# Performance work log

Hardware: AMD Instinct MI355X
Metric: run time of the kernel (lower is better)

The kernel has to match this reference:

```python
import jax, jax.numpy as jnp
import numpy as np

DIM = 4096
N_HEADS = 32
N_KV_HEADS = 8
HEAD_DIM = 128
EPS = 1e-6
SEQ = 2048
N_SEG = 4
SEG_LEN = SEQ // N_SEG


def setup_inputs() -> dict:
    key = jax.random.key(0)
    ks = jax.random.split(key, 6)
    s = 0.02
    x = jax.random.normal(ks[0], (1, SEQ, DIM), jnp.float32)
    wq = jax.random.normal(ks[1], (N_HEADS * HEAD_DIM, DIM), jnp.float32) * s
    wk = jax.random.normal(ks[2], (N_KV_HEADS * HEAD_DIM, DIM), jnp.float32) * s
    wv = jax.random.normal(ks[3], (N_KV_HEADS * HEAD_DIM, DIM), jnp.float32) * s
    wo = jax.random.normal(ks[4], (DIM, N_HEADS * HEAD_DIM), jnp.float32) * s
    q_norm_w = jnp.ones((HEAD_DIM,), jnp.float32)
    k_norm_w = jnp.ones((HEAD_DIM,), jnp.float32)
    # RoPE cache: [max_pos, head_dim//2, 2] = (cos, sin)
    inv_freq = 1.0 / (10000.0 ** (jnp.arange(0, HEAD_DIM // 2, dtype=jnp.float32) / (HEAD_DIM // 2)))
    t = jnp.arange(SEQ, dtype=jnp.float32)
    freqs = jnp.outer(t, inv_freq)  # [SEQ, hd/2]
    rope_cache = jnp.stack([jnp.cos(freqs), jnp.sin(freqs)], axis=-1)
    # packed varlen: 4 segments of 512, positions restart per segment
    positions = (jnp.arange(SEQ, dtype=jnp.int32) % SEG_LEN)[None, :]
    cu_seqlens = jnp.arange(N_SEG + 1, dtype=jnp.int32) * SEG_LEN
    return {"x": x, "wq": wq, "wk": wk, "wv": wv, "wo": wo,
            "q_norm_w": q_norm_w, "k_norm_w": k_norm_w,
            "rope_cache": rope_cache, "positions": positions,
            "cu_seqlens": cu_seqlens}


def _rms_norm(x, w):
    xf = x.astype(jnp.float32)
    var = jnp.mean(xf * xf, axis=-1, keepdims=True)
    return w * (xf * jax.lax.rsqrt(var + EPS))


def _apply_rope(x, rope_cache, positions):
    # x: [bs, S, h, hd]; rope_cache: [P, hd/2, 2]; positions: [bs, S]
    cs = rope_cache[positions]                    # [bs, S, hd/2, 2]
    cos = cs[..., 0][:, :, None, :]               # [bs, S, 1, hd/2]
    sin = cs[..., 1][:, :, None, :]
    half = x.shape[-1] // 2
    x1, x2 = x[..., :half], x[..., half:]
    return jnp.concatenate([x1 * cos - x2 * sin, x2 * cos + x1 * sin], axis=-1)


def reference(x, wq, wk, wv, wo, q_norm_w, k_norm_w, rope_cache, positions, cu_seqlens):
    bs, S, _ = x.shape
    n_rep = N_HEADS // N_KV_HEADS
    xq = (x @ wq.T).reshape(bs, S, N_HEADS, HEAD_DIM)
    xk = (x @ wk.T).reshape(bs, S, N_KV_HEADS, HEAD_DIM)
    xv = (x @ wv.T).reshape(bs, S, N_KV_HEADS, HEAD_DIM)
    xq = _rms_norm(xq, q_norm_w)
    xk = _rms_norm(xk, k_norm_w)
    xq = _apply_rope(xq, rope_cache, positions)
    xk = _apply_rope(xk, rope_cache, positions)
    # GQA: repeat kv heads
    xk = jnp.repeat(xk, n_rep, axis=2)
    xv = jnp.repeat(xv, n_rep, axis=2)
    q = xq.transpose(0, 2, 1, 3)  # [bs, h, S, hd]
    k = xk.transpose(0, 2, 1, 3)
    v = xv.transpose(0, 2, 1, 3)
    # varlen mask: causal within each packed segment
    idx = jnp.arange(S)
    seg = jnp.searchsorted(cu_seqlens, idx, side='right') - 1  # [S]
    mask = (seg[:, None] == seg[None, :]) & (idx[:, None] >= idx[None, :])
    scale = HEAD_DIM ** -0.5
    scores = jnp.einsum('bhqd,bhkd->bhqk', q, k) * scale
    scores = jnp.where(mask[None, None], scores, jnp.float32(-1e30))
    probs = jax.nn.softmax(scores, axis=-1)
    out = jnp.einsum('bhqk,bhkd->bhqd', probs, v)
    out = out.transpose(0, 2, 1, 3).reshape(bs, S, N_HEADS * HEAD_DIM)
    return out @ wo.T
```

## Files before the change

### kernel.cpp

```cpp
#include <hip/hip_runtime.h>

typedef __bf16 bf16_t;
typedef __bf16 bf16x8 __attribute__((ext_vector_type(8)));
typedef __bf16 bf16x4 __attribute__((ext_vector_type(4)));
typedef float f32x4 __attribute__((ext_vector_type(4)));

#define SEQL 2048
#define DIMM 4096
#define NH 32
#define NKV 8
#define HD 128

__device__ __forceinline__ void gl2lds16(const void* g, void* l) {
  __builtin_amdgcn_global_load_lds((__attribute__((address_space(1))) void*)g,
                                   (__attribute__((address_space(3))) void*)l,
                                   16, 0, 0);
}

__global__ __launch_bounds__(256) void cvt5_kernel(const float* __restrict__ s0,
                                                   const float* __restrict__ s1,
                                                   const float* __restrict__ s2,
                                                   const float* __restrict__ s3,
                                                   const float* __restrict__ s4,
                                                   bf16_t* __restrict__ dst) {
  const long base = (long)blockIdx.x * 4096;
  const float* s;
  long o;
  if (base < 8388608L)       { s = s0; o = base; }
  else if (base < 25165824L) { s = s1; o = base - 8388608L; }
  else if (base < 29360128L) { s = s2; o = base - 25165824L; }
  else if (base < 33554432L) { s = s3; o = base - 29360128L; }
  else                       { s = s4; o = base - 33554432L; }
  const long t4 = threadIdx.x * 4;
#pragma unroll
  for (int j = 0; j < 4; ++j) {
    const long e = t4 + j * 1024;
    float4 v = *(const float4*)(s + o + e);
    bf16x4 ov;
    ov[0] = (bf16_t)v.x; ov[1] = (bf16_t)v.y; ov[2] = (bf16_t)v.z; ov[3] = (bf16_t)v.w;
    *(bf16x4*)(dst + base + e) = ov;
  }
}

#define BK2 32
#define EPS 264
#define QSCALE (0.08838834764831845f * 1.4426950408889634f)
__global__ __launch_bounds__(512, 2) void gemm_qkv8(const bf16_t* __restrict__ A,
                                                    const bf16_t* __restrict__ B,
                                                    const float* __restrict__ qnw,
                                                    const float* __restrict__ knw,
                                                    const float* __restrict__ rope,
                                                    const int* __restrict__ pos,
                                                    bf16_t* __restrict__ Qb,
                                                    bf16_t* __restrict__ Kb,
                                                    bf16_t* __restrict__ Vb) {
  __shared__ __align__(16) bf16_t smem[65536];
  const int K = DIMM;
  const int NT = K / BK2;
  const int tid = threadIdx.x;
  const int lin = blockIdx.x;
  const int xcd = lin & 7, idx = lin >> 3;
  const int bm = (idx & 7) * 256;
  const int bn = ((idx >> 3) + xcd * 3) * 256;
  const int lane = tid & 63, wave = tid >> 6;
  const int wrow = wave >> 2, wcol = wave & 3;
  const int wm = wrow * 128, wn = wcol * 64;
  const int lr = lane & 15, quad = lane >> 4;
  const int swz = (quad ^ ((lr >> 1) & 3)) << 3;

  long asrc[2]; int adst[2];
#pragma unroll
  for (int c = 0; c < 2; ++c) {
    const int id = tid + 512 * c;
    asrc[c] = (long)(id >> 2) * K + (long)((((id & 3) ^ ((id >> 3) & 3)) << 3));
    adst[c] = id * 8;
  }
  const bf16_t* Abase = A + (long)bm * K;
  const bf16_t* Bbase = B + (long)bn * K;

  f32x4 acc[8][4];
#pragma unroll
  for (int mi = 0; mi < 8; ++mi)
#pragma unroll
    for (int ni = 0; ni < 4; ++ni)
      acc[mi][ni] = (f32x4){0.f, 0.f, 0.f, 0.f};

#define STAGE(t, c)                                                              \
  do {                                                                           \
    const int slot_ = (t) & 3;                                                   \
    const long k0_ = (long)(t) * BK2;                                            \
    gl2lds16(Abase + asrc[c] + k0_, smem + slot_ * 8192 + adst[c]);              \
    gl2lds16(Bbase + asrc[c] + k0_, smem + 32768 + slot_ * 8192 + adst[c]);      \
  } while (0)

  STAGE(0, 0); STAGE(0, 1); STAGE(1, 0); STAGE(1, 1);
  asm volatile("s_waitcnt vmcnt(4)" ::: "memory");
  __builtin_amdgcn_s_barrier();

  for (int t = 0; t < NT; ++t) {
    const bf16_t* As = smem + (t & 3) * 8192;
    const bf16_t* Bs = smem + 32768 + (t & 3) * 8192;
    bf16x8 af[4], bfr[4];
#pragma unroll
    for (int mi = 0; mi < 4; ++mi)
      af[mi] = *(const bf16x8*)&As[(wm + mi * 16 + lr) * 32 + swz];
#pragma unroll
    for (int ni = 0; ni < 4; ++ni)
      bfr[ni] = *(const bf16x8*)&Bs[(wn + ni * 16 + lr) * 32 + swz];
    if (t + 2 < NT) STAGE(t + 2, 0);
    __builtin_amdgcn_s_barrier();
    asm volatile("s_waitcnt lgkmcnt(0)" ::: "memory");
    __builtin_amdgcn_sched_barrier(0);
    __builtin_amdgcn_s_setprio(1);
#pragma unroll
    for (int mi = 0; mi < 4; ++mi)
#pragma unroll
      for (int ni = 0; ni < 4; ++ni)
        acc[mi][ni] = __builtin_amdgcn_mfma_f32_16x16x32_bf16(af[mi], bfr[ni], acc[mi][ni], 0, 0, 0);
    __builtin_amdgcn_s_setprio(0);
    __builtin_amdgcn_s_barrier();
#pragma unroll
    for (int mi = 0; mi < 4; ++mi)
      af[mi] = *(const bf16x8*)&As[(wm + 64 + mi * 16 + lr) * 32 + swz];
    if (t + 2 < NT) STAGE(t + 2, 1);
    __builtin_amdgcn_s_barrier();
    asm volatile("s_waitcnt lgkmcnt(0)" ::: "memory");
    __builtin_amdgcn_sched_barrier(0);
    __builtin_amdgcn_s_setprio(1);
#pragma unroll
    for (int mi = 0; mi < 4; ++mi)
#pragma unroll
      for (int ni = 0; ni < 4; ++ni)
        acc[4 + mi][ni] = __builtin_amdgcn_mfma_f32_16x16x32_bf16(af[mi], bfr[ni], acc[4 + mi][ni], 0, 0, 0);
    __builtin_amdgcn_s_setprio(0);
    if (t + 2 < NT) { asm volatile("s_waitcnt vmcnt(4)" ::: "memory"); }
    else            { asm volatile("s_waitcnt vmcnt(0)" ::: "memory"); }
    __builtin_amdgcn_s_barrier();
  }
#undef STAGE

  const bool isQ = bn < 4096;
  const bool isV = bn >= 5120;
#pragma unroll 1
  for (int half = 0; half < 2; ++half) {
    __syncthreads();
    if (wrow == half) {
#pragma unroll
      for (int mi = 0; mi < 8; ++mi)
#pragma unroll
        for (int ni = 0; ni < 4; ++ni)
#pragma unroll
          for (int r = 0; r < 4; ++r)
            smem[(mi * 16 + quad * 4 + r) * EPS + wn + ni * 16 + lr] = (bf16_t)acc[mi][ni][r];
    }
    __syncthreads();
    const int growb = bm + half * 128;
    if (!isV) {
      const int r = tid >> 2, hh = (tid >> 1) & 1, hf = tid & 1;
      const int cb = bn + hh * 128;
      const float* nwp = isQ ? qnw : knw;
      const float osc = isQ ? QSCALE : 1.0f;
      bf16_t* outp = isQ ? (Qb + (long)(cb >> 7) * SEQL * HD)
                         : (Kb + (long)((cb - 4096) >> 7) * SEQL * HD);
      bf16x8 rowv[16];
#pragma unroll
      for (int j = 0; j < 16; ++j) rowv[j] = *(const bf16x8*)&smem[r * EPS + hh * 128 + j * 8];
      float ss = 0.f;
#pragma unroll
      for (int j = 0; j < 16; ++j)
#pragma unroll
        for (int e = 0; e < 8; ++e) { const float f = (float)rowv[j][e]; ss += f * f; }
      const float sc = rsqrtf(ss * (1.0f / 128.0f) + 1e-6f) * osc;
      const int p = pos[growb + r];
      const float* rp = rope + p * 128;
      bf16_t obuf[64];
#pragma unroll
      for (int g = 0; g < 8; ++g) {
#pragma unroll
        for (int e = 0; e < 8; ++e) {
          const int i = g * 8 + e;
          const float2 cs = *(const float2*)(rp + 2 * i);
          const float nlo = (float)rowv[i >> 3][i & 7] * sc * nwp[i];
          const float nhi = (float)rowv[8 + (i >> 3)][i & 7] * sc * nwp[64 + i];
          obuf[i] = (bf16_t)(hf ? (nhi * cs.x + nlo * cs.y) : (nlo * cs.x - nhi * cs.y));
        }
      }
      bf16_t* op = outp + (long)(growb + r) * HD + hf * 64;
#pragma unroll
      for (int g = 0; g < 8; ++g) *(bf16x8*)(op + g * 8) = *(const bf16x8*)&obuf[g * 8];
    } else {
      const int d = tid & 127, q2 = tid >> 7;
      const int hh = q2 >> 1, shalf = q2 & 1;
      const int hv = ((bn - 5120) >> 7) + hh;
      bf16_t* vp = Vb + ((long)hv * HD + d) * SEQL + growb + shalf * 64;
#pragma unroll
      for (int grp = 0; grp < 8; ++grp) {
        bf16x8 tv;
#pragma unroll
        for (int e = 0; e < 8; ++e) tv[e] = smem[(shalf * 64 + grp * 8 + e) * EPS + hh * 128 + d];
        *(bf16x8*)(vp + grp * 8) = tv;
      }
    }
  }
}

template <typename CT>
__global__ __launch_bounds__(256, 3) void gemm_bt_kernel(const bf16_t* __restrict__ A,
                                                         const bf16_t* __restrict__ B,
                                                         CT* __restrict__ C,
                                                         int N, int K, int npanel) {
  __shared__ bf16_t lA[128 * 64];
  __shared__ bf16_t lB[128 * 64];
  const int tid = threadIdx.x;
  const int lin = blockIdx.x;
  const int xcd = lin & 7, idx = lin >> 3;
  const int bm = (idx & 15) * 128;
  const int bn = ((idx >> 4) + xcd * npanel) * 128;
  const int lane = tid & 63, wave = tid >> 6;
  const int wm = (wave >> 1) * 64, wn = (wave & 1) * 64;
  const int lr = lane & 15, quad = lane >> 4;

  f32x4 acc[4][4];
#pragma unroll
  for (int mi = 0; mi < 4; ++mi)
#pragma unroll
    for (int ni = 0; ni < 4; ++ni)
      acc[mi][ni] = (f32x4){0.f, 0.f, 0.f, 0.f};

  long soff[4];
#pragma unroll
  for (int c = 0; c < 4; ++c) {
    const int s = tid + 256 * c;
    soff[c] = (long)(s >> 3) * K + (((s & 7) ^ ((s >> 3) & 7)) << 3);
  }
  const bf16_t* Abase = A + (long)bm * K;
  const bf16_t* Bbase = B + (long)bn * K;

  for (int k0 = 0; k0 < K; k0 += 64) {
    __syncthreads();
#pragma unroll
    for (int c = 0; c < 4; ++c) {
      gl2lds16(Abase + soff[c] + k0, lA + (tid + 256 * c) * 8);
      gl2lds16(Bbase + soff[c] + k0, lB + (tid + 256 * c) * 8);
    }
    __syncthreads();
#pragma unroll
    for (int ks = 0; ks < 2; ++ks) {
      bf16x8 af[4], bfr[4];
#pragma unroll
      for (int mi = 0; mi < 4; ++mi)
        af[mi] = *(const bf16x8*)&lA[(wm + mi * 16 + lr) * 64 + ((((ks << 2) | quad) ^ (lr & 7)) << 3)];
#pragma unroll
      for (int ni = 0; ni < 4; ++ni)
        bfr[ni] = *(const bf16x8*)&lB[(wn + ni * 16 + lr) * 64 + ((((ks << 2) | quad) ^ (lr & 7)) << 3)];
#pragma unroll
      for (int mi = 0; mi < 4; ++mi)
#pragma unroll
        for (int ni = 0; ni < 4; ++ni)
          acc[mi][ni] = __builtin_amdgcn_mfma_f32_16x16x32_bf16(af[mi], bfr[ni], acc[mi][ni], 0, 0, 0);
    }
  }

#pragma unroll
  for (int mi = 0; mi < 4; ++mi) {
    const int row = bm + wm + mi * 16 + quad * 4;
#pragma unroll
    for (int ni = 0; ni < 4; ++ni) {
      const int col = bn + wn + ni * 16 + lr;
      CT* cp = C + (long)row * N + col;
#pragma unroll
      for (int r = 0; r < 4; ++r) cp[(long)r * N] = (CT)acc[mi][ni][r];
    }
  }
}

#define CK 64
#define PSTR 72
__global__ __launch_bounds__(256) void attn_kernel(const bf16_t* __restrict__ Q,
                                                   const bf16_t* __restrict__ Kt,
                                                   const bf16_t* __restrict__ Vt,
                                                   bf16_t* __restrict__ O) {
  __shared__ bf16_t lK[CK * 128];
  __shared__ bf16_t lV[144 * CK];
  __shared__ bf16_t lP[128 * PSTR];
  const int lin = blockIdx.x;
  const int qb = (lin < 256) ? (3 - (lin & 1)) : (lin & 1);
  const int gh = (lin >> 1) & 127;
  const int h = gh & 31, g = gh >> 5;
  const int hk = h >> 2;
  const int tid = threadIdx.x, lane = tid & 63, wave = tid >> 6;
  const int lr = lane & 15, quad = lane >> 4;
  const int s_base = g * 512 + qb * 128;

  if (tid < 128) {
    bf16x8 one8;
#pragma unroll
    for (int j = 0; j < 8; ++j) one8[j] = (bf16_t)1.0f;
    *(bf16x8*)&lV[128 * CK + tid * 8] = one8;
  }

  bf16x8 qf[2][4];
  const bf16_t* Qp = Q + ((long)h * SEQL + s_base + wave * 32 + lr) * HD + quad * 8;
#pragma unroll
  for (int mi = 0; mi < 2; ++mi)
#pragma unroll
    for (int ks = 0; ks < 4; ++ks)
      qf[mi][ks] = *(const bf16x8*)(Qp + mi * 16 * HD + ks * 32);

  f32x4 oacc[2][9];
#pragma unroll
  for (int mi = 0; mi < 2; ++mi)
#pragma unroll
    for (int di = 0; di < 9; ++di) oacc[mi][di] = (f32x4){0.f, 0.f, 0.f, 0.f};

  const int nchunk = 2 * qb + 2;
  for (int c = 0; c < nchunk; ++c) {
    __syncthreads();
    {
      const bf16_t* Kg = Kt + ((long)hk * SEQL + g * 512 + c * CK) * HD;
      const bf16_t* Vg = Vt + (long)hk * HD * SEQL + g * 512 + c * CK;
#pragma unroll
      for (int cc = 0; cc < 4; ++cc) {
        const int i = tid + 256 * cc;
        gl2lds16(Kg + (long)(i >> 4) * HD + (i & 15) * 8, lK + i * 8);
        gl2lds16(Vg + (long)(i >> 3) * SEQL + (i & 7) * 8, lV + i * 8);
      }
    }
    __syncthreads();

    f32x4 sv[2][4];
#pragma unroll
    for (int mi = 0; mi < 2; ++mi)
#pragma unroll
      for (int ni = 0; ni < 4; ++ni) sv[mi][ni] = (f32x4){0.f, 0.f, 0.f, 0.f};
#pragma unroll
    for (int ks = 0; ks < 4; ++ks) {
#pragma unroll
      for (int ni = 0; ni < 4; ++ni) {
        const bf16x8 kf = *(const bf16x8*)&lK[(ni * 16 + lr) * 128 + ks * 32 + quad * 8];
        sv[0][ni] = __builtin_amdgcn_mfma_f32_16x16x32_bf16(qf[0][ks], kf, sv[0][ni], 0, 0, 0);
        sv[1][ni] = __builtin_amdgcn_mfma_f32_16x16x32_bf16(qf[1][ks], kf, sv[1][ni], 0, 0, 0);
      }
    }

#pragma unroll
    for (int mi = 0; mi < 2; ++mi)
#pragma unroll
      for (int ni = 0; ni < 4; ++ni)
#pragma unroll
        for (int r = 0; r < 4; ++r) {
          const int colseg = c * CK + ni * 16 + lr;
          const int rowseg = qb * 128 + wave * 32 + mi * 16 + quad * 4 + r;
          float p = exp2f(sv[mi][ni][r]);
          p = (colseg > rowseg) ? 0.f : p;
          lP[(wave * 32 + mi * 16 + quad * 4 + r) * PSTR + ni * 16 + lr] = (bf16_t)p;
        }
    __syncthreads();

#pragma unroll
    for (int ks = 0; ks < 2; ++ks) {
      const bf16x8 pf0 = *(const bf16x8*)&lP[(wave * 32 + lr) * PSTR + ks * 32 + quad * 8];
      const bf16x8 pf1 = *(const bf16x8*)&lP[(wave * 32 + 16 + lr) * PSTR + ks * 32 + quad * 8];
#pragma unroll
      for (int di = 0; di < 9; ++di) {
        const bf16x8 vfr = *(const bf16x8*)&lV[(di * 16 + lr) * CK + ks * 32 + quad * 8];
        oacc[0][di] = __builtin_amdgcn_mfma_f32_16x16x32_bf16(pf0, vfr, oacc[0][di], 0, 0, 0);
        oacc[1][di] = __builtin_amdgcn_mfma_f32_16x16x32_bf16(pf1, vfr, oacc[1][di], 0, 0, 0);
      }
    }
  }

#pragma unroll
  for (int mi = 0; mi < 2; ++mi)
#pragma unroll
    for (int r = 0; r < 4; ++r) {
      const float inv = 1.0f / oacc[mi][8][r];
      const int row = s_base + wave * 32 + mi * 16 + quad * 4 + r;
      bf16_t* opp = O + (long)row * DIMM + h * HD + lr;
#pragma unroll
      for (int di = 0; di < 8; ++di) opp[di * 16] = (bf16_t)(oacc[mi][di][r] * inv);
    }
}

extern "C" void kernel_launch(void* const* d_in, const int* in_sizes, int n_in,
                              void* d_out, int out_size, void* d_ws, size_t ws_size,
                              hipStream_t stream) {
  (void)in_sizes; (void)n_in; (void)out_size; (void)ws_size;
  const float* x    = (const float*)d_in[0];
  const float* wq   = (const float*)d_in[1];
  const float* wk   = (const float*)d_in[2];
  const float* wv   = (const float*)d_in[3];
  const float* wo   = (const float*)d_in[4];
  const float* qnw  = (const float*)d_in[5];
  const float* knw  = (const float*)d_in[6];
  const float* rope = (const float*)d_in[7];
  const int*   pos  = (const int*)d_in[8];
  float* out = (float*)d_out;

  char* ws = (char*)d_ws;
  size_t off = 0;
  auto alloc = [&](size_t b) { char* p = ws + off; off += (b + 255) & ~(size_t)255; return p; };
  bf16_t* xb    = (bf16_t*)alloc((size_t)SEQL * DIMM * 2);
  bf16_t* wqkvb = (bf16_t*)alloc((size_t)DIMM * DIMM * 2);
  alloc((size_t)NKV * HD * DIMM * 2);
  alloc((size_t)NKV * HD * DIMM * 2);
  bf16_t* wob   = (bf16_t*)alloc((size_t)DIMM * DIMM * 2);
  bf16_t* Qb    = (bf16_t*)alloc((size_t)NH * SEQL * HD * 2);
  bf16_t* Kb    = (bf16_t*)alloc((size_t)NKV * SEQL * HD * 2);
  bf16_t* Vb    = (bf16_t*)alloc((size_t)NKV * SEQL * HD * 2);
  bf16_t* attnb = xb;

  cvt5_kernel<<<dim3(12288), 256, 0, stream>>>(x, wq, wk, wv, wo, xb);
  gemm_qkv8<<<dim3(192), 512, 0, stream>>>(xb, wqkvb, qnw, knw, rope, pos, Qb, Kb, Vb);
  attn_kernel<<<dim3(512), 256, 0, stream>>>(Qb, Kb, Vb, attnb);
  gemm_bt_kernel<float><<<dim3(512), 256, 0, stream>>>(attnb, wob, out, DIMM, DIMM, 4);
}
```

Before: 531.1 us.

## Retile fused QKV GEMM to 128x384 blocks for full CU occupancy

Changes the fused QKV projection tile from 256x256 to 128x384, which raises the grid from 192 to 256 blocks so every CU gets work on a 256-CU part. It reworks the LDS staging split, wave tiling and the normalize/RoPE epilogue to match: the epilogue now writes all accumulators at once and handles three 128-wide head groups in two passes. The intent is to remove the partially idle wave of blocks. The trade-off is lower arithmetic intensity per tile and a less balanced second epilogue pass.

```diff
diff --git a/kernel.cpp b/kernel.cpp
--- a/kernel.cpp
+++ b/kernel.cpp
@@ -43,7 +43,7 @@
 }
 
 #define BK2 32
-#define EPS 264
+#define EPSTR 392
 #define QSCALE (0.08838834764831845f * 1.4426950408889634f)
 __global__ __launch_bounds__(512, 2) void gemm_qkv8(const bf16_t* __restrict__ A,
                                                     const bf16_t* __restrict__ B,
@@ -60,54 +60,64 @@
   const int tid = threadIdx.x;
   const int lin = blockIdx.x;
   const int xcd = lin & 7, idx = lin >> 3;
-  const int bm = (idx & 7) * 256;
-  const int bn = ((idx >> 3) + xcd * 3) * 256;
+  const int bm = (idx & 15) * 128;
+  const int bn = ((idx >> 4) + xcd * 2) * 384;
   const int lane = tid & 63, wave = tid >> 6;
   const int wrow = wave >> 2, wcol = wave & 3;
-  const int wm = wrow * 128, wn = wcol * 64;
+  const int wm = wrow * 64, wn = wcol * 96;
   const int lr = lane & 15, quad = lane >> 4;
   const int swz = (quad ^ ((lr >> 1) & 3)) << 3;
 
-  long asrc[2]; int adst[2];
-#pragma unroll
-  for (int c = 0; c < 2; ++c) {
+  const int idA = tid;
+  const long srcA = (long)(idA >> 2) * K + (((idA & 3) ^ ((idA >> 3) & 3)) << 3);
+  const int dstA = idA * 8;
+  long srcB[3]; int dstB[3];
+#pragma unroll
+  for (int c = 0; c < 3; ++c) {
     const int id = tid + 512 * c;
-    asrc[c] = (long)(id >> 2) * K + (long)((((id & 3) ^ ((id >> 3) & 3)) << 3));
-    adst[c] = id * 8;
+    srcB[c] = (long)(id >> 2) * K + (((id & 3) ^ ((id >> 3) & 3)) << 3);
+    dstB[c] = id * 8;
   }
   const bf16_t* Abase = A + (long)bm * K;
   const bf16_t* Bbase = B + (long)bn * K;
 
-  f32x4 acc[8][4];
-#pragma unroll
-  for (int mi = 0; mi < 8; ++mi)
-#pragma unroll
-    for (int ni = 0; ni < 4; ++ni)
+  f32x4 acc[4][6];
+#pragma unroll
+  for (int mi = 0; mi < 4; ++mi)
+#pragma unroll
+    for (int ni = 0; ni < 6; ++ni)
       acc[mi][ni] = (f32x4){0.f, 0.f, 0.f, 0.f};
 
-#define STAGE(t, c)                                                              \
+#define STAGE_A(t)                                                               \
   do {                                                                           \
-    const int slot_ = (t) & 3;                                                   \
+    const int sl_ = (t) & 3;                                                     \
     const long k0_ = (long)(t) * BK2;                                            \
-    gl2lds16(Abase + asrc[c] + k0_, smem + slot_ * 8192 + adst[c]);              \
-    gl2lds16(Bbase + asrc[c] + k0_, smem + 32768 + slot_ * 8192 + adst[c]);      \
+    gl2lds16(Abase + srcA + k0_, smem + sl_ * 4096 + dstA);                      \
+    gl2lds16(Bbase + srcB[0] + k0_, smem + 16384 + sl_ * 12288 + dstB[0]);       \
   } while (0)
-
-  STAGE(0, 0); STAGE(0, 1); STAGE(1, 0); STAGE(1, 1);
+#define STAGE_B(t)                                                               \
+  do {                                                                           \
+    const int sl_ = (t) & 3;                                                     \
+    const long k0_ = (long)(t) * BK2;                                            \
+    gl2lds16(Bbase + srcB[1] + k0_, smem + 16384 + sl_ * 12288 + dstB[1]);       \
+    gl2lds16(Bbase + srcB[2] + k0_, smem + 16384 + sl_ * 12288 + dstB[2]);       \
+  } while (0)
+
+  STAGE_A(0); STAGE_B(0); STAGE_A(1); STAGE_B(1);
   asm volatile("s_waitcnt vmcnt(4)" ::: "memory");
   __builtin_amdgcn_s_barrier();
 
   for (int t = 0; t < NT; ++t) {
-    const bf16_t* As = smem + (t & 3) * 8192;
-    const bf16_t* Bs = smem + 32768 + (t & 3) * 8192;
-    bf16x8 af[4], bfr[4];
+    const bf16_t* As = smem + (t & 3) * 4096;
+    const bf16_t* Bs = smem + 16384 + (t & 3) * 12288;
+    bf16x8 af[4], bfr[6];
 #pragma unroll
     for (int mi = 0; mi < 4; ++mi)
       af[mi] = *(const bf16x8*)&As[(wm + mi * 16 + lr) * 32 + swz];
 #pragma unroll
-    for (int ni = 0; ni < 4; ++ni)
+    for (int ni = 0; ni < 3; ++ni)
       bfr[ni] = *(const bf16x8*)&Bs[(wn + ni * 16 + lr) * 32 + swz];
-    if (t + 2 < NT) STAGE(t + 2, 0);
+    if (t + 2 < NT) STAGE_A(t + 2);
     __builtin_amdgcn_s_barrier();
     asm volatile("s_waitcnt lgkmcnt(0)" ::: "memory");
     __builtin_amdgcn_sched_barrier(0);
@@ -115,14 +125,14 @@
 #pragma unroll
     for (int mi = 0; mi < 4; ++mi)
 #pragma unroll
-      for (int ni = 0; ni < 4; ++ni)
+      for (int ni = 0; ni < 3; ++ni)
         acc[mi][ni] = __builtin_amdgcn_mfma_f32_16x16x32_bf16(af[mi], bfr[ni], acc[mi][ni], 0, 0, 0);
     __builtin_amdgcn_s_setprio(0);
     __builtin_amdgcn_s_barrier();
 #pragma unroll
-    for (int mi = 0; mi < 4; ++mi)
-      af[mi] = *(const bf16x8*)&As[(wm + 64 + mi * 16 + lr) * 32 + swz];
-    if (t + 2 < NT) STAGE(t + 2, 1);
+    for (int ni = 3; ni < 6; ++ni)
+      bfr[ni] = *(const bf16x8*)&Bs[(wn + ni * 16 + lr) * 32 + swz];
+    if (t + 2 < NT) STAGE_B(t + 2);
     __builtin_amdgcn_s_barrier();
     asm volatile("s_waitcnt lgkmcnt(0)" ::: "memory");
     __builtin_amdgcn_sched_barrier(0);
@@ -130,74 +140,75 @@
 #pragma unroll
     for (int mi = 0; mi < 4; ++mi)
 #pragma unroll
-      for (int ni = 0; ni < 4; ++ni)
-        acc[4 + mi][ni] = __builtin_amdgcn_mfma_f32_16x16x32_bf16(af[mi], bfr[ni], acc[4 + mi][ni], 0, 0, 0);
+      for (int ni = 3; ni < 6; ++ni)
+        acc[mi][ni] = __builtin_amdgcn_mfma_f32_16x16x32_bf16(af[mi], bfr[ni], acc[mi][ni], 0, 0, 0);
     __builtin_amdgcn_s_setprio(0);
     if (t + 2 < NT) { asm volatile("s_waitcnt vmcnt(4)" ::: "memory"); }
     else            { asm volatile("s_waitcnt vmcnt(0)" ::: "memory"); }
     __builtin_amdgcn_s_barrier();
   }
-#undef STAGE
-
-  const bool isQ = bn < 4096;
-  const bool isV = bn >= 5120;
+#undef STAGE_A
+#undef STAGE_B
+
+  __syncthreads();
+#pragma unroll
+  for (int mi = 0; mi < 4; ++mi)
+#pragma unroll
+    for (int ni = 0; ni < 6; ++ni)
+#pragma unroll
+      for (int r = 0; r < 4; ++r)
+        smem[(wm + mi * 16 + quad * 4 + r) * EPSTR + wn + ni * 16 + lr] = (bf16_t)acc[mi][ni][r];
+  __syncthreads();
+
 #pragma unroll 1
-  for (int half = 0; half < 2; ++half) {
-    __syncthreads();
-    if (wrow == half) {
-#pragma unroll
-      for (int mi = 0; mi < 8; ++mi)
-#pragma unroll
-        for (int ni = 0; ni < 4; ++ni)
-#pragma unroll
-          for (int r = 0; r < 4; ++r)
-            smem[(mi * 16 + quad * 4 + r) * EPS + wn + ni * 16 + lr] = (bf16_t)acc[mi][ni][r];
-    }
-    __syncthreads();
-    const int growb = bm + half * 128;
-    if (!isV) {
-      const int r = tid >> 2, hh = (tid >> 1) & 1, hf = tid & 1;
-      const int cb = bn + hh * 128;
+  for (int pass = 0; pass < 2; ++pass) {
+    const int hh = (pass == 0) ? (tid >> 8) : 2;
+    if (pass == 1 && tid >= 256) break;
+    const int tl = tid & 255;
+    const int col0 = bn + hh * 128;
+    if (col0 < 5120) {
+      const bool isQ = col0 < 4096;
+      const int r = tl >> 1, hf = tl & 1;
+      const bf16_t* rowp = smem + r * EPSTR + hh * 128;
+      float ss = 0.f;
+#pragma unroll
+      for (int j = 0; j < 16; ++j) {
+        const bf16x8 v = *(const bf16x8*)&rowp[j * 8];
+#pragma unroll
+        for (int e = 0; e < 8; ++e) { const float f = (float)v[e]; ss += f * f; }
+      }
+      const float sc = rsqrtf(ss * (1.0f / 128.0f) + 1e-6f) * (isQ ? QSCALE : 1.0f);
       const float* nwp = isQ ? qnw : knw;
-      const float osc = isQ ? QSCALE : 1.0f;
-      bf16_t* outp = isQ ? (Qb + (long)(cb >> 7) * SEQL * HD)
-                         : (Kb + (long)((cb - 4096) >> 7) * SEQL * HD);
-      bf16x8 rowv[16];
-#pragma unroll
-      for (int j = 0; j < 16; ++j) rowv[j] = *(const bf16x8*)&smem[r * EPS + hh * 128 + j * 8];
-      float ss = 0.f;
-#pragma unroll
-      for (int j = 0; j < 16; ++j)
-#pragma unroll
-        for (int e = 0; e < 8; ++e) { const float f = (float)rowv[j][e]; ss += f * f; }
-      const float sc = rsqrtf(ss * (1.0f / 128.0f) + 1e-6f) * osc;
-      const int p = pos[growb + r];
+      const int p = pos[bm + r];
       const float* rp = rope + p * 128;
-      bf16_t obuf[64];
+      bf16_t* op = (isQ ? (Qb + (long)(col0 >> 7) * SEQL * HD)
+                        : (Kb + (long)((col0 - 4096) >> 7) * SEQL * HD))
+                   + (long)(bm + r) * HD + hf * 64;
 #pragma unroll
       for (int g = 0; g < 8; ++g) {
+        const bf16x8 lo = *(const bf16x8*)&rowp[g * 8];
+        const bf16x8 hi = *(const bf16x8*)&rowp[64 + g * 8];
+        bf16x8 ov;
 #pragma unroll
         for (int e = 0; e < 8; ++e) {
           const int i = g * 8 + e;
           const float2 cs = *(const float2*)(rp + 2 * i);
-          const float nlo = (float)rowv[i >> 3][i & 7] * sc * nwp[i];
-          const float nhi = (float)rowv[8 + (i >> 3)][i & 7] * sc * nwp[64 + i];
-          obuf[i] = (bf16_t)(hf ? (nhi * cs.x + nlo * cs.y) : (nlo * cs.x - nhi * cs.y));
+          const float nlo = (float)lo[e] * sc * nwp[i];
+          const float nhi = (float)hi[e] * sc * nwp[64 + i];
+          ov[e] = (bf16_t)(hf ? (nhi * cs.x + nlo * cs.y) : (nlo * cs.x - nhi * cs.y));
         }
-      }
-      bf16_t* op = outp + (long)(growb + r) * HD + hf * 64;
-#pragma unroll
-      for (int g = 0; g < 8; ++g) *(bf16x8*)(op + g * 8) = *(const bf16x8*)&obuf[g * 8];
+        *(bf16x8*)(op + g * 8) = ov;
+      }
     } else {
-      const int d = tid & 127, q2 = tid >> 7;
-      const int hh = q2 >> 1, shalf = q2 & 1;
-      const int hv = ((bn - 5120) >> 7) + hh;
-      bf16_t* vp = Vb + ((long)hv * HD + d) * SEQL + growb + shalf * 64;
+      const int d = tl & 127, shalf = tl >> 7;
+      const int hv = (col0 - 5120) >> 7;
+      bf16_t* vp = Vb + ((long)hv * HD + d) * SEQL + bm + shalf * 64;
 #pragma unroll
       for (int grp = 0; grp < 8; ++grp) {
         bf16x8 tv;
 #pragma unroll
-        for (int e = 0; e < 8; ++e) tv[e] = smem[(shalf * 64 + grp * 8 + e) * EPS + hh * 128 + d];
+        for (int e = 0; e < 8; ++e)
+          tv[e] = smem[(shalf * 64 + grp * 8 + e) * EPSTR + hh * 128 + d];
         *(bf16x8*)(vp + grp * 8) = tv;
       }
     }
@@ -411,7 +422,7 @@
   bf16_t* attnb = xb;
 
   cvt5_kernel<<<dim3(12288), 256, 0, stream>>>(x, wq, wk, wv, wo, xb);
-  gemm_qkv8<<<dim3(192), 512, 0, stream>>>(xb, wqkvb, qnw, knw, rope, pos, Qb, Kb, Vb);
+  gemm_qkv8<<<dim3(256), 512, 0, stream>>>(xb, wqkvb, qnw, knw, rope, pos, Qb, Kb, Vb);
   attn_kernel<<<dim3(512), 256, 0, stream>>>(Qb, Kb, Vb, attnb);
   gemm_bt_kernel<float><<<dim3(512), 256, 0, stream>>>(attnb, wob, out, DIMM, DIMM, 4);
 }
```

Result: faster. 440.0 us (-17.2%).
